# Kernel optimization log

Measured on AMD Instinct MI355X. Metric: run time of the kernel, lower is better.

The kernel has to match this reference:

```python
import jax, jax.numpy as jnp
import numpy as np

IN_F = 256
OUT_F = 256
ALPHA = 0.2  # LeakyReLU negative slope
NEG_INF = -9e15


def setup_inputs() -> dict:
    key = jax.random.key(0)
    k_h, k_adj, k_w, k_a = jax.random.split(key, 4)
    N = 8192
    h = jax.random.normal(k_h, (N, IN_F), dtype=jnp.float32)
    adj = jax.random.randint(k_adj, (N, N), 0, 2, dtype=jnp.int32)
    # xavier_uniform with gain=1.414
    gain = 1.414
    limW = gain * np.sqrt(6.0 / (IN_F + OUT_F))
    W = jax.random.uniform(k_w, (IN_F, OUT_F), minval=-limW, maxval=limW, dtype=jnp.float32)
    lima = gain * np.sqrt(6.0 / (2 * OUT_F + 1))
    a = jax.random.uniform(k_a, (2 * OUT_F, 1), minval=-lima, maxval=lima, dtype=jnp.float32)
    return {"h": h, "adj": adj, "W": W, "a": a}


def reference(h, adj, W, a):
    # Wh: [N, F]
    Wh = h @ W
    # The original materializes [N, N, 2F] concat pairs; equivalently
    # e[i, j] = leakyrelu(Wh[i] . a[:F] + Wh[j] . a[F:])
    a1 = a[:OUT_F, 0]  # [F]
    a2 = a[OUT_F:, 0]  # [F]
    s1 = Wh @ a1       # [N]
    s2 = Wh @ a2       # [N]
    e = jax.nn.leaky_relu(s1[:, None] + s2[None, :], negative_slope=ALPHA)  # [N, N]
    att = jnp.where(adj > 0, e, NEG_INF)
    att = jax.nn.softmax(att, axis=1)
    # dropout p=0.0 (eval) -> identity
    h_prime = att @ Wh  # [N, F]
    return jax.nn.elu(h_prime)  # concat=True path
```

## Files before the change

### kernel.cpp

```cpp
#include <hip/hip_runtime.h>

#define NN 8192
#define FF 256
#define PST 136

typedef _Float16 h8 __attribute__((ext_vector_type(8)));
typedef _Float16 h4 __attribute__((ext_vector_type(4)));
typedef float    f4 __attribute__((ext_vector_type(4)));
typedef int      i4v __attribute__((ext_vector_type(4)));

__device__ __forceinline__ unsigned fenc(float x) {
  unsigned u = __float_as_uint(x);
  return (u & 0x80000000u) ? ~u : (u | 0x80000000u);
}
__device__ __forceinline__ float fdec(unsigned e) {
  unsigned u = (e & 0x80000000u) ? (e ^ 0x80000000u) : ~e;
  return __uint_as_float(u);
}

__device__ __forceinline__ void sync_lds() {
  __builtin_amdgcn_s_waitcnt(0xc07f);
  __builtin_amdgcn_s_barrier();
}

__global__ __launch_bounds__(256) void k_wh(
    const float* __restrict__ h, const float* __restrict__ W,
    const float* __restrict__ a, _Float16* __restrict__ wfrag,
    float* __restrict__ s1, _Float16* __restrict__ s2h,
    unsigned* __restrict__ s2maxe) {
  __shared__ float hs[16 * 256];
  __shared__ _Float16 whs[16 * 264];
  const int t = threadIdx.x;
  const int r0 = blockIdx.x * 16;
#pragma unroll
  for (int i = 0; i < 4; ++i) {
    int idx = i * 1024 + t * 4;
    *(f4*)&hs[idx] = *(const f4*)&h[(size_t)r0 * 256 + idx];
  }
  __syncthreads();
  const int lane = t & 63;
  const int wv = t >> 6;
  const int rg = wv * 4;
  const int c4 = lane * 4;
  float acc[4][4];
#pragma unroll
  for (int i = 0; i < 4; ++i)
#pragma unroll
    for (int k = 0; k < 4; ++k) acc[i][k] = 0.f;
  f4 w[8];
#pragma unroll
  for (int i = 0; i < 8; ++i) w[i] = *(const f4*)&W[i * 256 + c4];
  for (int f = 0; f < 256; f += 8) {
    f4 nw[8];
    if (f < 248) {
#pragma unroll
      for (int i = 0; i < 8; ++i) nw[i] = *(const f4*)&W[(f + 8 + i) * 256 + c4];
    }
#pragma unroll
    for (int i = 0; i < 4; ++i) {
      f4 h0 = *(const f4*)&hs[(rg + i) * 256 + f];
      f4 h1 = *(const f4*)&hs[(rg + i) * 256 + f + 4];
#pragma unroll
      for (int k = 0; k < 4; ++k)
        acc[i][k] += h0[0]*w[0][k] + h0[1]*w[1][k] + h0[2]*w[2][k] + h0[3]*w[3][k]
                   + h1[0]*w[4][k] + h1[1]*w[5][k] + h1[2]*w[6][k] + h1[3]*w[7][k];
    }
    if (f < 248) {
#pragma unroll
      for (int i = 0; i < 8; ++i) w[i] = nw[i];
    }
  }
  float a1v[4], a2v[4];
#pragma unroll
  for (int k = 0; k < 4; ++k) { a1v[k] = a[c4 + k]; a2v[k] = a[256 + c4 + k]; }
#pragma unroll
  for (int i = 0; i < 4; ++i) {
    h4 hh;
    float p1 = 0.f, p2 = 0.f;
#pragma unroll
    for (int k = 0; k < 4; ++k) {
      hh[k] = (_Float16)acc[i][k];
      p1 += acc[i][k] * a1v[k];
      p2 += acc[i][k] * a2v[k];
    }
    *(h4*)&whs[(rg + i) * 264 + c4] = hh;
#pragma unroll
    for (int off = 32; off; off >>= 1) {
      p1 += __shfl_xor(p1, off);
      p2 += __shfl_xor(p2, off);
    }
    if (lane == 0) {
      const int r = r0 + rg + i;
      s1[r] = p1;
      s2h[r] = (_Float16)p2;
      atomicMax(s2maxe, fenc(p2));
    }
  }
  __syncthreads();
  {
    const int kt = blockIdx.x >> 1;
    const int hb = blockIdx.x & 1;
    const int lp = hb * 32 + (t & 31);
    const int kb = ((t & 31) >> 4) * 8;
    const int m16e = t & 15;
#pragma unroll
    for (int p = 0; p < 2; ++p) {
      const int n = (t >> 5) + p * 8;
      h8 v;
#pragma unroll
      for (int j = 0; j < 8; ++j) v[j] = whs[(kb + j) * 264 + n * 16 + m16e];
      *(h8*)&wfrag[(((size_t)kt * 16 + n) << 9) + lp * 8] = v;
    }
  }
}

__global__ __launch_bounds__(512, 4) void k_gat(
    const int* __restrict__ adj, const _Float16* __restrict__ wfrag,
    const float* __restrict__ s1g, const _Float16* __restrict__ s2h,
    const unsigned* __restrict__ s2maxe,
    float* __restrict__ o0, float* __restrict__ o1,
    float* __restrict__ lbuf) {
  __shared__ _Float16 P[2][32 * PST];
  __shared__ _Float16 s2l[4096];
  const int t = threadIdx.x;
  const int lane = t & 63;
  const int w = t >> 6;
  const int q = lane >> 4;
  const int m16 = lane & 15;
  const int rt = (int)blockIdx.x >> 1;
  const int kh = (int)blockIdx.x & 1;
  const int r0 = rt * 32;

  ((h8*)s2l)[t] = ((const h8*)(s2h + kh * 4096))[t];

  const int srow = 4 * w + q;
  const float s2m = fdec(*s2maxe);
  const float s1r = s1g[r0 + srow];
  const float u0 = s1r + s2m;
  const float mi = fmaxf(u0, 0.2f * u0);
  const float s1mi = s1r - mi;

  f4 acc[2][2];
#pragma unroll
  for (int m = 0; m < 2; ++m)
#pragma unroll
    for (int n = 0; n < 2; ++n)
#pragma unroll
      for (int e = 0; e < 4; ++e) acc[m][n][e] = 0.f;
  float lsum = 0.f;

  const int* adjp = adj + (size_t)(r0 + srow) * NN + kh * 4096 + m16 * 8;
  __syncthreads();

  i4v c0 = *(const i4v*)(adjp);
  i4v c1 = *(const i4v*)(adjp + 4);

  for (int p = 0; p < 32; ++p) {
    const _Float16* wfb =
        wfrag + ((((size_t)(kh * 128 + p * 4)) * 16 + 2 * w) << 9) + lane * 8;
    h8 bb[8];
#pragma unroll
    for (int ks = 0; ks < 4; ++ks) {
      bb[2 * ks]     = *(const h8*)(wfb + ks * 8192);
      bb[2 * ks + 1] = *(const h8*)(wfb + ks * 8192 + 512);
    }
    i4v n0 = c0, n1 = c1;
    if (p < 31) {
      n0 = *(const i4v*)(adjp + (p + 1) * 128);
      n1 = *(const i4v*)(adjp + (p + 1) * 128 + 4);
    }
    const h8 s2c = *(const h8*)&s2l[p * 128 + m16 * 8];
    h8 pa;
#pragma unroll
    for (int j = 0; j < 8; ++j) {
      const float s2v = (float)s2c[j];
      const float u = s1r + s2v;
      const float arg = s1mi + s2v - 0.8f * fminf(u, 0.f);
      const int msk = (j < 4) ? c0[j] : c1[j - 4];
      const float pv = (msk > 0) ? __expf(arg) : 0.f;
      lsum += pv;
      pa[j] = (_Float16)pv;
    }
    _Float16* Pb = &P[p & 1][0];
    *(h8*)&Pb[srow * PST + m16 * 8] = pa;
    sync_lds();
#pragma unroll
    for (int ks = 0; ks < 4; ++ks) {
      const h8 A0 = *(const h8*)&Pb[m16 * PST + ks * 32 + q * 8];
      const h8 A1 = *(const h8*)&Pb[(16 + m16) * PST + ks * 32 + q * 8];
      acc[0][0] = __builtin_amdgcn_mfma_f32_16x16x32_f16(A0, bb[2*ks],   acc[0][0], 0, 0, 0);
      acc[0][1] = __builtin_amdgcn_mfma_f32_16x16x32_f16(A0, bb[2*ks+1], acc[0][1], 0, 0, 0);
      acc[1][0] = __builtin_amdgcn_mfma_f32_16x16x32_f16(A1, bb[2*ks],   acc[1][0], 0, 0, 0);
      acc[1][1] = __builtin_amdgcn_mfma_f32_16x16x32_f16(A1, bb[2*ks+1], acc[1][1], 0, 0, 0);
    }
    c0 = n0; c1 = n1;
  }

  lsum += __shfl_xor(lsum, 1);
  lsum += __shfl_xor(lsum, 2);
  lsum += __shfl_xor(lsum, 4);
  lsum += __shfl_xor(lsum, 8);
  if (m16 == 0) lbuf[kh * NN + r0 + srow] = lsum;

  float* ob = kh ? o1 : o0;
#pragma unroll
  for (int m = 0; m < 2; ++m)
#pragma unroll
    for (int n = 0; n < 2; ++n)
#pragma unroll
      for (int v = 0; v < 4; ++v)
        ob[(size_t)(r0 + m * 16 + q * 4 + v) * FF + w * 32 + n * 16 + m16] =
            acc[m][n][v];
}

__global__ __launch_bounds__(256) void k_fin(
    float* __restrict__ out, const float* __restrict__ o1,
    const float* __restrict__ lbuf) {
  const int t = threadIdx.x;
  const int row = blockIdx.x * 16 + (t >> 4);
  const int c0 = (t & 15) * 16;
  const float linv = 1.0f / (lbuf[row] + lbuf[NN + row]);
#pragma unroll
  for (int i = 0; i < 4; ++i) {
    f4 v0 = *(const f4*)&out[(size_t)row * FF + c0 + i * 4];
    f4 v1 = *(const f4*)&o1[(size_t)row * FF + c0 + i * 4];
    f4 o;
#pragma unroll
    for (int e = 0; e < 4; ++e) {
      float x = (v0[e] + v1[e]) * linv;
      o[e] = (x > 0.f) ? x : (__expf(x) - 1.f);
    }
    *(f4*)&out[(size_t)row * FF + c0 + i * 4] = o;
  }
}

extern "C" void kernel_launch(void* const* d_in, const int* in_sizes, int n_in,
                              void* d_out, int out_size, void* d_ws, size_t ws_size,
                              hipStream_t stream) {
  const float* h   = (const float*)d_in[0];
  const int*   adj = (const int*)d_in[1];
  const float* W   = (const float*)d_in[2];
  const float* a   = (const float*)d_in[3];
  float* out = (float*)d_out;

  char* ws = (char*)d_ws;
  _Float16* wfrag = (_Float16*)ws;
  float*    o1    = (float*)(ws + (4u << 20));
  float*    lbuf  = (float*)(ws + (12u << 20));
  unsigned* s2me  = (unsigned*)(ws + (12u << 20) + 65536);
  float*    s1    = (float*)(ws + (12u << 20) + 65600);
  _Float16* s2h   = (_Float16*)(ws + (12u << 20) + 65600 + 32768);

  hipMemsetAsync(s2me, 0, 4, stream);
  k_wh<<<512, 256, 0, stream>>>(h, W, a, wfrag, s1, s2h, s2me);
  k_gat<<<512, 512, 0, stream>>>(adj, wfrag, s1, s2h, s2me, out, o1, lbuf);
  k_fin<<<512, 256, 0, stream>>>(out, o1, lbuf);
}
```

Before: 502.2 us.

## Use 64-row tiles with a 4-way key split in attention kernel

Measured after the change: 504.6 us. About the same (+0.5%).

```diff
diff --git a/kernel.cpp b/kernel.cpp
--- a/kernel.cpp
+++ b/kernel.cpp
@@ -119,92 +119,119 @@
     const float* __restrict__ s1g, const _Float16* __restrict__ s2h,
     const unsigned* __restrict__ s2maxe,
     float* __restrict__ o0, float* __restrict__ o1,
+    float* __restrict__ o2, float* __restrict__ o3,
     float* __restrict__ lbuf) {
-  __shared__ _Float16 P[2][32 * PST];
-  __shared__ _Float16 s2l[4096];
+  __shared__ _Float16 P[2][64 * PST];
+  __shared__ _Float16 s2l[2048];
   const int t = threadIdx.x;
   const int lane = t & 63;
   const int w = t >> 6;
   const int q = lane >> 4;
   const int m16 = lane & 15;
-  const int rt = (int)blockIdx.x >> 1;
-  const int kh = (int)blockIdx.x & 1;
-  const int r0 = rt * 32;
-
-  ((h8*)s2l)[t] = ((const h8*)(s2h + kh * 4096))[t];
-
-  const int srow = 4 * w + q;
+  const int rt = (int)blockIdx.x >> 2;
+  const int kq = (int)blockIdx.x & 3;
+  const int r0 = rt * 64;
+
+  if (t < 256) ((h8*)s2l)[t] = ((const h8*)(s2h + kq * 2048))[t];
+
+  const int srA = 8 * w + q;
+  const int srB = srA + 4;
   const float s2m = fdec(*s2maxe);
-  const float s1r = s1g[r0 + srow];
-  const float u0 = s1r + s2m;
-  const float mi = fmaxf(u0, 0.2f * u0);
-  const float s1mi = s1r - mi;
-
-  f4 acc[2][2];
-#pragma unroll
-  for (int m = 0; m < 2; ++m)
+  const float s1A = s1g[r0 + srA];
+  const float s1B = s1g[r0 + srB];
+  const float uA0 = s1A + s2m, uB0 = s1B + s2m;
+  const float miA = fmaxf(uA0, 0.2f * uA0);
+  const float miB = fmaxf(uB0, 0.2f * uB0);
+  const float sAmi = s1A - miA, sBmi = s1B - miB;
+
+  f4 acc[4][2];
+#pragma unroll
+  for (int m = 0; m < 4; ++m)
 #pragma unroll
     for (int n = 0; n < 2; ++n)
 #pragma unroll
       for (int e = 0; e < 4; ++e) acc[m][n][e] = 0.f;
-  float lsum = 0.f;
-
-  const int* adjp = adj + (size_t)(r0 + srow) * NN + kh * 4096 + m16 * 8;
+  float lsA = 0.f, lsB = 0.f;
+
+  const int* adjA = adj + (size_t)(r0 + srA) * NN + kq * 2048 + m16 * 8;
+  const int* adjB = adj + (size_t)(r0 + srB) * NN + kq * 2048 + m16 * 8;
   __syncthreads();
 
-  i4v c0 = *(const i4v*)(adjp);
-  i4v c1 = *(const i4v*)(adjp + 4);
-
-  for (int p = 0; p < 32; ++p) {
+  i4v a0 = *(const i4v*)(adjA);
+  i4v a1 = *(const i4v*)(adjA + 4);
+  i4v b0 = *(const i4v*)(adjB);
+  i4v b1 = *(const i4v*)(adjB + 4);
+
+  for (int p = 0; p < 16; ++p) {
     const _Float16* wfb =
-        wfrag + ((((size_t)(kh * 128 + p * 4)) * 16 + 2 * w) << 9) + lane * 8;
+        wfrag + ((((size_t)(kq * 64 + p * 4)) * 16 + 2 * w) << 9) + lane * 8;
     h8 bb[8];
 #pragma unroll
     for (int ks = 0; ks < 4; ++ks) {
       bb[2 * ks]     = *(const h8*)(wfb + ks * 8192);
       bb[2 * ks + 1] = *(const h8*)(wfb + ks * 8192 + 512);
     }
-    i4v n0 = c0, n1 = c1;
-    if (p < 31) {
-      n0 = *(const i4v*)(adjp + (p + 1) * 128);
-      n1 = *(const i4v*)(adjp + (p + 1) * 128 + 4);
+    i4v na0 = a0, na1 = a1, nb0 = b0, nb1 = b1;
+    if (p < 15) {
+      na0 = *(const i4v*)(adjA + (p + 1) * 128);
+      na1 = *(const i4v*)(adjA + (p + 1) * 128 + 4);
+      nb0 = *(const i4v*)(adjB + (p + 1) * 128);
+      nb1 = *(const i4v*)(adjB + (p + 1) * 128 + 4);
     }
     const h8 s2c = *(const h8*)&s2l[p * 128 + m16 * 8];
-    h8 pa;
+    h8 pA, pB;
 #pragma unroll
     for (int j = 0; j < 8; ++j) {
       const float s2v = (float)s2c[j];
-      const float u = s1r + s2v;
-      const float arg = s1mi + s2v - 0.8f * fminf(u, 0.f);
-      const int msk = (j < 4) ? c0[j] : c1[j - 4];
-      const float pv = (msk > 0) ? __expf(arg) : 0.f;
-      lsum += pv;
-      pa[j] = (_Float16)pv;
+      const int mA = (j < 4) ? a0[j] : a1[j - 4];
+      const int mB = (j < 4) ? b0[j] : b1[j - 4];
+      const float uA = s1A + s2v;
+      const float uB = s1B + s2v;
+      const float argA = sAmi + s2v - 0.8f * fminf(uA, 0.f);
+      const float argB = sBmi + s2v - 0.8f * fminf(uB, 0.f);
+      const float pvA = (mA > 0) ? __expf(argA) : 0.f;
+      const float pvB = (mB > 0) ? __expf(argB) : 0.f;
+      lsA += pvA; pA[j] = (_Float16)pvA;
+      lsB += pvB; pB[j] = (_Float16)pvB;
     }
     _Float16* Pb = &P[p & 1][0];
-    *(h8*)&Pb[srow * PST + m16 * 8] = pa;
+    *(h8*)&Pb[srA * PST + m16 * 8] = pA;
+    *(h8*)&Pb[srB * PST + m16 * 8] = pB;
     sync_lds();
 #pragma unroll
     for (int ks = 0; ks < 4; ++ks) {
-      const h8 A0 = *(const h8*)&Pb[m16 * PST + ks * 32 + q * 8];
+      const h8 A0 = *(const h8*)&Pb[(     m16) * PST + ks * 32 + q * 8];
       const h8 A1 = *(const h8*)&Pb[(16 + m16) * PST + ks * 32 + q * 8];
+      const h8 A2 = *(const h8*)&Pb[(32 + m16) * PST + ks * 32 + q * 8];
+      const h8 A3 = *(const h8*)&Pb[(48 + m16) * PST + ks * 32 + q * 8];
       acc[0][0] = __builtin_amdgcn_mfma_f32_16x16x32_f16(A0, bb[2*ks],   acc[0][0], 0, 0, 0);
       acc[0][1] = __builtin_amdgcn_mfma_f32_16x16x32_f16(A0, bb[2*ks+1], acc[0][1], 0, 0, 0);
       acc[1][0] = __builtin_amdgcn_mfma_f32_16x16x32_f16(A1, bb[2*ks],   acc[1][0], 0, 0, 0);
       acc[1][1] = __builtin_amdgcn_mfma_f32_16x16x32_f16(A1, bb[2*ks+1], acc[1][1], 0, 0, 0);
-    }
-    c0 = n0; c1 = n1;
-  }
-
-  lsum += __shfl_xor(lsum, 1);
-  lsum += __shfl_xor(lsum, 2);
-  lsum += __shfl_xor(lsum, 4);
-  lsum += __shfl_xor(lsum, 8);
-  if (m16 == 0) lbuf[kh * NN + r0 + srow] = lsum;
-
-  float* ob = kh ? o1 : o0;
-#pragma unroll
-  for (int m = 0; m < 2; ++m)
+      acc[2][0] = __builtin_amdgcn_mfma_f32_16x16x32_f16(A2, bb[2*ks],   acc[2][0], 0, 0, 0);
+      acc[2][1] = __builtin_amdgcn_mfma_f32_16x16x32_f16(A2, bb[2*ks+1], acc[2][1], 0, 0, 0);
+      acc[3][0] = __builtin_amdgcn_mfma_f32_16x16x32_f16(A3, bb[2*ks],   acc[3][0], 0, 0, 0);
+      acc[3][1] = __builtin_amdgcn_mfma_f32_16x16x32_f16(A3, bb[2*ks+1], acc[3][1], 0, 0, 0);
+    }
+    a0 = na0; a1 = na1; b0 = nb0; b1 = nb1;
+  }
+
+  lsA += __shfl_xor(lsA, 1);
+  lsA += __shfl_xor(lsA, 2);
+  lsA += __shfl_xor(lsA, 4);
+  lsA += __shfl_xor(lsA, 8);
+  lsB += __shfl_xor(lsB, 1);
+  lsB += __shfl_xor(lsB, 2);
+  lsB += __shfl_xor(lsB, 4);
+  lsB += __shfl_xor(lsB, 8);
+  if (m16 == 0) {
+    lbuf[kq * NN + r0 + srA] = lsA;
+    lbuf[kq * NN + r0 + srB] = lsB;
+  }
+
+  float* ob = (kq == 0) ? o0 : (kq == 1) ? o1 : (kq == 2) ? o2 : o3;
+#pragma unroll
+  for (int m = 0; m < 4; ++m)
 #pragma unroll
     for (int n = 0; n < 2; ++n)
 #pragma unroll
@@ -215,19 +242,23 @@
 
 __global__ __launch_bounds__(256) void k_fin(
     float* __restrict__ out, const float* __restrict__ o1,
+    const float* __restrict__ o2, const float* __restrict__ o3,
     const float* __restrict__ lbuf) {
   const int t = threadIdx.x;
   const int row = blockIdx.x * 16 + (t >> 4);
   const int c0 = (t & 15) * 16;
-  const float linv = 1.0f / (lbuf[row] + lbuf[NN + row]);
+  const float linv = 1.0f / (lbuf[row] + lbuf[NN + row] +
+                             lbuf[2 * NN + row] + lbuf[3 * NN + row]);
 #pragma unroll
   for (int i = 0; i < 4; ++i) {
     f4 v0 = *(const f4*)&out[(size_t)row * FF + c0 + i * 4];
     f4 v1 = *(const f4*)&o1[(size_t)row * FF + c0 + i * 4];
+    f4 v2 = *(const f4*)&o2[(size_t)row * FF + c0 + i * 4];
+    f4 v3 = *(const f4*)&o3[(size_t)row * FF + c0 + i * 4];
     f4 o;
 #pragma unroll
     for (int e = 0; e < 4; ++e) {
-      float x = (v0[e] + v1[e]) * linv;
+      float x = (v0[e] + v1[e] + v2[e] + v3[e]) * linv;
       o[e] = (x > 0.f) ? x : (__expf(x) - 1.f);
     }
     *(f4*)&out[(size_t)row * FF + c0 + i * 4] = o;
@@ -246,13 +277,15 @@
   char* ws = (char*)d_ws;
   _Float16* wfrag = (_Float16*)ws;
   float*    o1    = (float*)(ws + (4u << 20));
-  float*    lbuf  = (float*)(ws + (12u << 20));
-  unsigned* s2me  = (unsigned*)(ws + (12u << 20) + 65536);
-  float*    s1    = (float*)(ws + (12u << 20) + 65600);
-  _Float16* s2h   = (_Float16*)(ws + (12u << 20) + 65600 + 32768);
+  float*    o2    = (float*)(ws + (12u << 20));
+  float*    o3    = (float*)(ws + (20u << 20));
+  float*    lbuf  = (float*)(ws + (28u << 20));
+  unsigned* s2me  = (unsigned*)(ws + (28u << 20) + 131072);
+  float*    s1    = (float*)(ws + (28u << 20) + 131072 + 64);
+  _Float16* s2h   = (_Float16*)(ws + (28u << 20) + 131072 + 64 + 32768);
 
   hipMemsetAsync(s2me, 0, 4, stream);
   k_wh<<<512, 256, 0, stream>>>(h, W, a, wfrag, s1, s2h, s2me);
-  k_gat<<<512, 512, 0, stream>>>(adj, wfrag, s1, s2h, s2me, out, o1, lbuf);
-  k_fin<<<512, 256, 0, stream>>>(out, o1, lbuf);
-}
+  k_gat<<<512, 512, 0, stream>>>(adj, wfrag, s1, s2h, s2me, out, o1, o2, o3, lbuf);
+  k_fin<<<512, 256, 0, stream>>>(out, o1, o2, o3, lbuf);
+}
```
